# Kernel tuning notes

Measured on AMD Instinct MI355X. Metric: run time of the kernel, lower is better.

The kernel has to match this reference:

```python
import jax, jax.numpy as jnp
import numpy as np

N = 50000      # nodes
E = 800000     # edges
IN = 128       # in_channels
HID = 32       # hidden_channels (per-head dim)
HEADS = 4
HC = HEADS * HID  # 128
OUT = 16       # classes
B = 64         # graphs in batch


def setup_inputs() -> dict:
    key = jax.random.key(0)
    ks = jax.random.split(key, 32)
    def nrm(k, shp, scale):
        return (jax.random.normal(k, shp, jnp.float32) * scale).astype(jnp.float32)
    inp = {}
    inp["x"] = nrm(ks[0], (N, IN), 1.0)
    inp["edge_index"] = jax.random.randint(ks[1], (2, E), 0, N, dtype=jnp.int32)
    inp["edge_attr"] = nrm(ks[2], (E, HID), 1.0)
    inp["batch"] = jnp.sort(jax.random.randint(ks[3], (N,), 0, B, dtype=jnp.int32))
    s_in = IN ** -0.5
    s_hc = HC ** -0.5
    s_hid = HID ** -0.5
    # conv1: lin_query/key/value (IN->HC, bias), lin_edge (HID->HC, no bias), lin_skip (IN->HC, bias)
    inp["wq1"] = nrm(ks[4], (IN, HC), s_in);  inp["bq1"] = jnp.zeros((HC,), jnp.float32)
    inp["wk1"] = nrm(ks[5], (IN, HC), s_in);  inp["bk1"] = jnp.zeros((HC,), jnp.float32)
    inp["wv1"] = nrm(ks[6], (IN, HC), s_in);  inp["bv1"] = jnp.zeros((HC,), jnp.float32)
    inp["we1"] = nrm(ks[7], (HID, HC), s_hid)
    inp["ws1"] = nrm(ks[8], (IN, HC), s_in);  inp["bs1"] = jnp.zeros((HC,), jnp.float32)
    # conv2: input dim HC
    inp["wq2"] = nrm(ks[9], (HC, HC), s_hc);  inp["bq2"] = jnp.zeros((HC,), jnp.float32)
    inp["wk2"] = nrm(ks[10], (HC, HC), s_hc); inp["bk2"] = jnp.zeros((HC,), jnp.float32)
    inp["wv2"] = nrm(ks[11], (HC, HC), s_hc); inp["bv2"] = jnp.zeros((HC,), jnp.float32)
    inp["we2"] = nrm(ks[12], (HID, HC), s_hid)
    inp["ws2"] = nrm(ks[13], (HC, HC), s_hc); inp["bs2"] = jnp.zeros((HC,), jnp.float32)
    # final classifier
    inp["wlin"] = nrm(ks[14], (HC, OUT), s_hc); inp["blin"] = jnp.zeros((OUT,), jnp.float32)
    return inp


def _tconv(x, src, tgt, ea, wq, bq, wk, bk, wv, bv, we, ws, bs):
    """PyG TransformerConv (concat=True, root_weight=True, eval/no dropout)."""
    qn = x @ wq + bq          # [N, HC]
    kn = x @ wk + bk
    vn = x @ wv + bv
    e = ea @ we               # [E, HC] edge embedding (added to key and value)
    q = qn[tgt].reshape(E, HEADS, HID)
    k = (kn[src] + e).reshape(E, HEADS, HID)
    v = (vn[src] + e).reshape(E, HEADS, HID)
    alpha = (q * k).sum(-1) / np.float32(np.sqrt(HID))   # [E, HEADS]
    # segment softmax over target node
    m = jax.ops.segment_max(alpha, tgt, num_segments=N)  # [N, HEADS]
    a = jnp.exp(alpha - m[tgt])
    den = jax.ops.segment_sum(a, tgt, num_segments=N)
    a = a / den[tgt]
    agg = jax.ops.segment_sum(a[:, :, None] * v, tgt, num_segments=N)  # [N, HEADS, HID]
    return agg.reshape(N, HC) + (x @ ws + bs)


def reference(x, edge_index, edge_attr, batch,
              wq1, bq1, wk1, bk1, wv1, bv1, we1, ws1, bs1,
              wq2, bq2, wk2, bk2, wv2, bv2, we2, ws2, bs2,
              wlin, blin):
    src, tgt = edge_index[0], edge_index[1]
    h = jax.nn.elu(_tconv(x, src, tgt, edge_attr, wq1, bq1, wk1, bk1, wv1, bv1, we1, ws1, bs1))
    h = jax.nn.elu(_tconv(h, src, tgt, edge_attr, wq2, bq2, wk2, bk2, wv2, bv2, we2, ws2, bs2))
    # global mean pool over graphs
    s = jax.ops.segment_sum(h, batch, num_segments=B)                    # [B, HC]
    cnt = jax.ops.segment_sum(jnp.ones((N,), jnp.float32), batch, num_segments=B)
    pooled = s / jnp.maximum(cnt, 1.0)[:, None]
    logits = pooled @ wlin + blin
    return jax.nn.log_softmax(logits, axis=-1)
```

## Files before the change

### kernel.cpp

```cpp
#include <hip/hip_runtime.h>
#include <hip/hip_fp16.h>

#define N_NODES 50000
#define N_EDGES 800000
#define IN_C 128
#define HID 32
#define HC 128
#define OUT_C 16
#define NGRAPH 64
#define PNB 125
#define TPB 2

typedef __attribute__((ext_vector_type(8))) _Float16 half8;
typedef __attribute__((ext_vector_type(4))) _Float16 half4v;
typedef __attribute__((ext_vector_type(2))) _Float16 half2v;
typedef __attribute__((ext_vector_type(4))) float floatx4;

__global__ void k_hist(const int* __restrict__ tgt, int* __restrict__ deg) {
  int i = blockIdx.x * blockDim.x + threadIdx.x;
  if (i < N_EDGES) atomicAdd(&deg[tgt[i]], 1);
}

__global__ __launch_bounds__(1024) void k_scan(const int* __restrict__ deg,
                                               int* __restrict__ offs,
                                               int* __restrict__ cursor) {
  __shared__ int wsum[16];
  __shared__ int carry_s;
  int lane = threadIdx.x & 63, wid = threadIdx.x >> 6;
  if (threadIdx.x == 0) { carry_s = 0; offs[0] = 0; }
  __syncthreads();
  for (int base = 0; base < N_NODES; base += 1024) {
    int i = base + threadIdx.x;
    int v = (i < N_NODES) ? deg[i] : 0;
    int x = v;
#pragma unroll
    for (int off = 1; off < 64; off <<= 1) {
      int t = __shfl_up(x, off, 64);
      if (lane >= off) x += t;
    }
    if (lane == 63) wsum[wid] = x;
    __syncthreads();
    if (wid == 0 && lane < 16) {
      int s = wsum[lane];
#pragma unroll
      for (int off = 1; off < 16; off <<= 1) {
        int t = __shfl_up(s, off, 64);
        if (lane >= off) s += t;
      }
      wsum[lane] = s;
    }
    __syncthreads();
    int add = (wid > 0 ? wsum[wid - 1] : 0) + carry_s;
    int incl = x + add;
    if (i < N_NODES) { offs[i + 1] = incl; cursor[i] = incl - v; }
    __syncthreads();
    if (threadIdx.x == 1023) carry_s = incl;
    __syncthreads();
  }
}

__global__ void k_scatter(const int* __restrict__ src, const int* __restrict__ tgt,
                          int* __restrict__ cursor, int* __restrict__ srcs,
                          int* __restrict__ eids) {
  int i = blockIdx.x * blockDim.x + threadIdx.x;
  if (i < N_EDGES) {
    int pos = atomicAdd(&cursor[tgt[i]], 1);
    srcs[pos] = src[i];
    eids[pos] = i;
  }
}

__global__ __launch_bounds__(256) void k_perm_ea(const int* __restrict__ eids,
                                                 const float* __restrict__ ea,
                                                 _Float16* __restrict__ eac) {
  int i = blockIdx.x * 32 + (threadIdx.x >> 3);
  int c = (threadIdx.x & 7) * 4;
  if (i < N_EDGES) {
    float4 v = *(const float4*)&ea[(size_t)eids[i] * HID + c];
    half4v h = {(_Float16)v.x, (_Float16)v.y, (_Float16)v.z, (_Float16)v.w};
    *(half4v*)&eac[(size_t)i * HID + c] = h;
  }
}

__global__ void k_conv_x(const float* __restrict__ x, _Float16* __restrict__ x16) {
  int i = blockIdx.x * 256 + threadIdx.x;
  if (i * 8 < N_NODES * HC) {
    float4 v0 = *(const float4*)&x[i * 8];
    float4 v1 = *(const float4*)&x[i * 8 + 4];
    half8 h = {(_Float16)v0.x, (_Float16)v0.y, (_Float16)v0.z, (_Float16)v0.w,
               (_Float16)v1.x, (_Float16)v1.y, (_Float16)v1.z, (_Float16)v1.w};
    *(half8*)&x16[i * 8] = h;
  }
}

__global__ __launch_bounds__(128) void k_conv_w(
    const float* __restrict__ wq, const float* __restrict__ wk,
    const float* __restrict__ wv, const float* __restrict__ ws,
    _Float16* __restrict__ wt) {
  int g = blockIdx.x;
  int k = threadIdx.x;
  const float* w = (g < 128) ? wq : (g < 256) ? wk : (g < 384) ? wv : ws;
  int c = g & 127;
  wt[g * HC + k] = (_Float16)w[k * HC + c];
}

__global__ __launch_bounds__(128) void k_fold_p(const float* __restrict__ wq,
                                                const float* __restrict__ bq,
                                                const float* __restrict__ we,
                                                _Float16* __restrict__ wt,
                                                float* __restrict__ bp) {
  int c = blockIdx.x;
  int k = threadIdx.x;
  int hb = (c >> 5) << 5, j = c & 31;
  float s = 0.f;
#pragma unroll
  for (int d = 0; d < 32; ++d)
    s = fmaf(wq[k * HC + hb + d], we[j * HC + hb + d], s);
  wt[(size_t)(512 + c) * HC + k] = (_Float16)s;
  if (k == 0) {
    float b = 0.f;
    for (int d = 0; d < 32; ++d) b = fmaf(bq[hb + d], we[j * HC + hb + d], b);
    bp[c] = b;
  }
}

__global__ __launch_bounds__(256) void k_gemm(
    const _Float16* __restrict__ ain,
    const _Float16* __restrict__ wt,
    const float* __restrict__ bq, const float* __restrict__ bk,
    const float* __restrict__ bv, const float* __restrict__ bs,
    const float* __restrict__ bp,
    __half* __restrict__ qn16, _Float16* __restrict__ kv16,
    float* __restrict__ sk, __half* __restrict__ p16) {
  __shared__ _Float16 Bs[128][132];
  int tid = threadIdx.x;
  int wv = tid >> 6, lane = tid & 63;
  int quad = lane >> 4, l16 = lane & 15;
  int cb = blockIdx.y;

#pragma unroll
  for (int i = 0; i < 8; ++i) {
    int chunk = i * 256 + tid;
    int col = chunk >> 4, kc16 = chunk & 15;
    half8 b = *(const half8*)&wt[(size_t)(cb * 128 + col) * HC + kc16 * 8];
    *(half8*)&Bs[col][kc16 * 8] = b;
  }

  int r0 = blockIdx.x * 128 + wv * 32;
  half8 A[2][4];
#pragma unroll
  for (int m = 0; m < 2; ++m) {
    int arow = min(r0 + m * 16 + l16, N_NODES - 1);
#pragma unroll
    for (int kc = 0; kc < 4; ++kc)
      A[m][kc] = *(const half8*)&ain[(size_t)arow * HC + kc * 32 + quad * 8];
  }
  floatx4 acc[8][2];
#pragma unroll
  for (int ct = 0; ct < 8; ++ct) {
    acc[ct][0] = (floatx4){0.f, 0.f, 0.f, 0.f};
    acc[ct][1] = (floatx4){0.f, 0.f, 0.f, 0.f};
  }
  __syncthreads();

#pragma unroll
  for (int ct = 0; ct < 8; ++ct) {
#pragma unroll
    for (int kc = 0; kc < 4; ++kc) {
      half8 B = *(const half8*)&Bs[ct * 16 + l16][kc * 32 + quad * 8];
      acc[ct][0] = __builtin_amdgcn_mfma_f32_16x16x32_f16(A[0][kc], B, acc[ct][0], 0, 0, 0);
      acc[ct][1] = __builtin_amdgcn_mfma_f32_16x16x32_f16(A[1][kc], B, acc[ct][1], 0, 0, 0);
    }
  }

  const float* bias = (cb == 0) ? bq : (cb == 1) ? bk : (cb == 2) ? bv
                    : (cb == 3) ? bs : bp;
#pragma unroll
  for (int ct = 0; ct < 8; ++ct) {
    int lc = (ct << 4) + l16;
    float b = bias[lc];
#pragma unroll
    for (int m = 0; m < 2; ++m) {
#pragma unroll
      for (int reg = 0; reg < 4; ++reg) {
        int row = r0 + m * 16 + quad * 4 + reg;
        if (row < N_NODES) {
          float val = acc[ct][m][reg] + b;
          if (cb == 0) qn16[(size_t)row * HC + lc] = __float2half(val);
          else if (cb == 1) kv16[(size_t)row * 256 + lc] = (_Float16)val;
          else if (cb == 2) kv16[(size_t)row * 256 + 128 + lc] = (_Float16)val;
          else if (cb == 3) sk[(size_t)row * HC + lc] = val;
          else p16[(size_t)row * HC + lc] = __float2half(val);
        }
      }
    }
  }
}

__device__ __forceinline__ float dot8(half8 a, half8 b, float c) {
#if __has_builtin(__builtin_amdgcn_fdot2)
#pragma unroll
  for (int i = 0; i < 4; ++i) {
    half2v x = {a[2 * i], a[2 * i + 1]};
    half2v y = {b[2 * i], b[2 * i + 1]};
    c = __builtin_amdgcn_fdot2(x, y, c, false);
  }
#else
#pragma unroll
  for (int i = 0; i < 8; ++i) c = fmaf((float)a[i], (float)b[i], c);
#endif
  return c;
}

__device__ __forceinline__ float quad_red(float x) {
  int b = __builtin_amdgcn_update_dpp(0, __float_as_int(x), 0xB1, 0xF, 0xF, true);
  float y = x + __int_as_float(b);
  int c2 = __builtin_amdgcn_update_dpp(0, __float_as_int(y), 0x4E, 0xF, 0xF, true);
  return y + __int_as_float(c2);
}

__global__ __launch_bounds__(128) void k_edge_attn(
    const int* __restrict__ offs, const int* __restrict__ srcs,
    const _Float16* __restrict__ eac,
    const _Float16* __restrict__ qn, const _Float16* __restrict__ kv,
    const float* __restrict__ sk,
    const _Float16* __restrict__ pn, const float* __restrict__ we,
    float* __restrict__ out, _Float16* __restrict__ o16) {
  int lane = threadIdx.x & 63;
  int wv_ = threadIdx.x >> 6;
  int t = blockIdx.x * TPB + wv_;
  int g = lane >> 4;
  int p = lane & 15;
  int f0 = p << 3;
  int jd0 = (p & 3) << 3;

  half8 qh = *(const half8*)&qn[(size_t)t * HC + f0];
  half8 ph = *(const half8*)&pn[(size_t)t * HC + ((p >> 2) << 5) + jd0];

  int e0 = offs[t], e1 = offs[t + 1];
  const float inv_sqrt = 0.17677669529663687f;
  float den = 0.f;
  float acc[8], tac[8];
#pragma unroll
  for (int i = 0; i < 8; ++i) { acc[i] = 0.f; tac[i] = 0.f; }

  int sl = (e0 < e1) ? srcs[min(e0 + (lane & 15), e1 - 1)] : 0;
  for (int base = e0; base < e1; base += 16) {
    int cnt = e1 - base;
    half8 K[4], V[4], E[4];
#pragma unroll
    for (int i = 0; i < 4; ++i) {
      int j = 4 * g + i;
      int jc = min(j, cnt - 1);
      int s = __shfl(sl, jc, 64);
      const _Float16* kvp = &kv[(size_t)s * 256];
      K[i] = *(const half8*)&kvp[f0];
      V[i] = *(const half8*)&kvp[128 + f0];
      E[i] = *(const half8*)&eac[(size_t)(base + jc) * HID + jd0];
    }
    int nb = base + 16;
    int sl_n = (nb < e1) ? srcs[min(nb + (lane & 15), e1 - 1)] : 0;
#pragma unroll
    for (int i = 0; i < 4; ++i) {
      int j = 4 * g + i;
      float part = dot8(qh, K[i], 0.f);
      part = dot8(ph, E[i], part);
      part = quad_red(part);
      float w = (j < cnt) ? __expf(part * inv_sqrt) : 0.f;
      den += w;
#pragma unroll
      for (int q2 = 0; q2 < 8; ++q2) {
        acc[q2] = fmaf(w, (float)V[i][q2], acc[q2]);
        tac[q2] = fmaf(w, (float)E[i][q2], tac[q2]);
      }
    }
    sl = sl_n;
  }

#pragma unroll
  for (int i = 0; i < 8; ++i) {
    acc[i] += __shfl_xor(acc[i], 16, 64); acc[i] += __shfl_xor(acc[i], 32, 64);
    tac[i] += __shfl_xor(tac[i], 16, 64); tac[i] += __shfl_xor(tac[i], 32, 64);
  }
  den += __shfl_xor(den, 16, 64);
  den += __shfl_xor(den, 32, 64);

  __shared__ float tl[TPB][16][9];
  if (g == 0) {
#pragma unroll
    for (int i = 0; i < 8; ++i) tl[wv_][p][i] = tac[i];
  }
  float fx[8];
#pragma unroll
  for (int i = 0; i < 8; ++i) fx[i] = 0.f;
  int r = (p & 12) + g;
#pragma unroll
  for (int u = 0; u < 8; ++u) {
    float tv = tl[wv_][r][u];
    int j = (g << 3) + u;
    const float4* wr = (const float4*)&we[j * HC + f0];
    float4 w0 = wr[0], w1 = wr[1];
    fx[0] = fmaf(tv, w0.x, fx[0]); fx[1] = fmaf(tv, w0.y, fx[1]);
    fx[2] = fmaf(tv, w0.z, fx[2]); fx[3] = fmaf(tv, w0.w, fx[3]);
    fx[4] = fmaf(tv, w1.x, fx[4]); fx[5] = fmaf(tv, w1.y, fx[5]);
    fx[6] = fmaf(tv, w1.z, fx[6]); fx[7] = fmaf(tv, w1.w, fx[7]);
  }
#pragma unroll
  for (int i = 0; i < 8; ++i) {
    fx[i] += __shfl_xor(fx[i], 16, 64);
    fx[i] += __shfl_xor(fx[i], 32, 64);
  }

  if (g == 0) {
    float rd = (e1 > e0) ? (1.0f / den) : 0.f;
    const float4* skp = (const float4*)&sk[(size_t)t * HC + f0];
    float4 sa = skp[0], sb = skp[1];
    float o[8];
    o[0] = fmaf(acc[0] + fx[0], rd, sa.x);
    o[1] = fmaf(acc[1] + fx[1], rd, sa.y);
    o[2] = fmaf(acc[2] + fx[2], rd, sa.z);
    o[3] = fmaf(acc[3] + fx[3], rd, sa.w);
    o[4] = fmaf(acc[4] + fx[4], rd, sb.x);
    o[5] = fmaf(acc[5] + fx[5], rd, sb.y);
    o[6] = fmaf(acc[6] + fx[6], rd, sb.z);
    o[7] = fmaf(acc[7] + fx[7], rd, sb.w);
#pragma unroll
    for (int i = 0; i < 8; ++i) o[i] = o[i] > 0.f ? o[i] : __expf(o[i]) - 1.f;
    *(float4*)&out[(size_t)t * HC + f0] = (float4){o[0], o[1], o[2], o[3]};
    *(float4*)&out[(size_t)t * HC + f0 + 4] = (float4){o[4], o[5], o[6], o[7]};
    half8 v16 = {(_Float16)o[0], (_Float16)o[1], (_Float16)o[2], (_Float16)o[3],
                 (_Float16)o[4], (_Float16)o[5], (_Float16)o[6], (_Float16)o[7]};
    *(half8*)&o16[(size_t)t * HC + f0] = v16;
  }
}

__global__ __launch_bounds__(128) void k_pool_sum(const float* __restrict__ h,
                                                  const int* __restrict__ batch,
                                                  float* __restrict__ psum) {
  int c = threadIdx.x;
  int n0 = blockIdx.x * PNB;
  int n1 = n0 + PNB;
  float acc = 0.f;
  int curb = batch[n0];
  for (int n = n0; n < n1; ++n) {
    int b = batch[n];
    if (b != curb) {
      atomicAdd(&psum[curb * HC + c], acc);
      acc = 0.f;
      curb = b;
    }
    acc += h[n * HC + c];
  }
  atomicAdd(&psum[curb * HC + c], acc);
}

__global__ __launch_bounds__(1024) void k_classify(const float* __restrict__ psum,
                                                   const int* __restrict__ batch,
                                                   const float* __restrict__ wlin,
                                                   const float* __restrict__ blin,
                                                   float* __restrict__ out) {
  int tid = threadIdx.x;
  int b = tid >> 4, o = tid & 15;
  int lo = 0, hi = N_NODES;
  while (lo < hi) { int mid = (lo + hi) >> 1; if (batch[mid] < b) lo = mid + 1; else hi = mid; }
  int start = lo;
  lo = 0; hi = N_NODES;
  while (lo < hi) { int mid = (lo + hi) >> 1; if (batch[mid] <= b) lo = mid + 1; else hi = mid; }
  float cnt = fmaxf((float)(lo - start), 1.0f);
  float dot = 0.f;
  for (int d = 0; d < HC; ++d) dot = fmaf(psum[b * HC + d], wlin[d * OUT_C + o], dot);
  float acc = dot / cnt + blin[o];
  float mx = acc;
#pragma unroll
  for (int off = 8; off > 0; off >>= 1) mx = fmaxf(mx, __shfl_xor(mx, off, 64));
  float ex = __expf(acc - mx);
  float sum = ex;
#pragma unroll
  for (int off = 8; off > 0; off >>= 1) sum += __shfl_xor(sum, off, 64);
  out[tid] = acc - mx - logf(sum);
}

extern "C" void kernel_launch(void* const* d_in, const int* in_sizes, int n_in,
                              void* d_out, int out_size, void* d_ws, size_t ws_size,
                              hipStream_t stream) {
  const float* x = (const float*)d_in[0];
  const int* ei = (const int*)d_in[1];
  const float* ea = (const float*)d_in[2];
  const int* batch = (const int*)d_in[3];
  const float* wq1 = (const float*)d_in[4];  const float* bq1 = (const float*)d_in[5];
  const float* wk1 = (const float*)d_in[6];  const float* bk1 = (const float*)d_in[7];
  const float* wv1 = (const float*)d_in[8];  const float* bv1 = (const float*)d_in[9];
  const float* we1 = (const float*)d_in[10];
  const float* ws1 = (const float*)d_in[11]; const float* bs1 = (const float*)d_in[12];
  const float* wq2 = (const float*)d_in[13]; const float* bq2 = (const float*)d_in[14];
  const float* wk2 = (const float*)d_in[15]; const float* bk2 = (const float*)d_in[16];
  const float* wv2 = (const float*)d_in[17]; const float* bv2 = (const float*)d_in[18];
  const float* we2 = (const float*)d_in[19];
  const float* ws2 = (const float*)d_in[20]; const float* bs2 = (const float*)d_in[21];
  const float* wlin = (const float*)d_in[22]; const float* blin = (const float*)d_in[23];

  const int* srcI = ei;
  const int* tgtI = ei + N_EDGES;

  char* wsb = (char*)d_ws;
  size_t off = 0;
  auto alloc = [&](size_t bytes) -> void* {
    void* ptr = wsb + off;
    off += (bytes + 255) & ~(size_t)255;
    return ptr;
  };
  __half* qn16 = (__half*)alloc((size_t)N_NODES * HC * 2);
  _Float16* kv16 = (_Float16*)alloc((size_t)N_NODES * 256 * 2);
  __half* p16  = (__half*)alloc((size_t)N_NODES * HC * 2);
  float* sk = (float*)alloc((size_t)N_NODES * HC * 4);
  float* h  = (float*)alloc((size_t)N_NODES * HC * 4);
  _Float16* in16 = (_Float16*)alloc((size_t)N_NODES * HC * 2);
  _Float16* wt1 = (_Float16*)alloc((size_t)640 * HC * 2);
  _Float16* wt2 = (_Float16*)alloc((size_t)640 * HC * 2);
  float* bp1 = (float*)alloc((size_t)HC * 4);
  float* bp2 = (float*)alloc((size_t)HC * 4);
  float* psum = (float*)alloc((size_t)NGRAPH * HC * 4);
  int* deg    = (int*)alloc((size_t)N_NODES * 4);
  int* offs   = (int*)alloc((size_t)(N_NODES + 1) * 4);
  int* cursor = (int*)alloc((size_t)N_NODES * 4);
  int* srcs   = (int*)alloc((size_t)N_EDGES * 4);
  int* eids   = (int*)alloc((size_t)N_EDGES * 4);
  _Float16* eac = (_Float16*)alloc((size_t)N_EDGES * HID * 2);

  hipMemsetAsync(deg, 0, (size_t)N_NODES * 4, stream);
  k_hist<<<(N_EDGES + 255) / 256, 256, 0, stream>>>(tgtI, deg);
  k_scan<<<1, 1024, 0, stream>>>(deg, offs, cursor);
  k_scatter<<<(N_EDGES + 255) / 256, 256, 0, stream>>>(srcI, tgtI, cursor, srcs, eids);
  k_perm_ea<<<N_EDGES / 32, 256, 0, stream>>>(eids, ea, eac);

  k_conv_x<<<(N_NODES * HC / 8 + 255) / 256, 256, 0, stream>>>(x, in16);
  k_conv_w<<<512, 128, 0, stream>>>(wq1, wk1, wv1, ws1, wt1);
  k_conv_w<<<512, 128, 0, stream>>>(wq2, wk2, wv2, ws2, wt2);
  k_fold_p<<<128, 128, 0, stream>>>(wq1, bq1, we1, wt1, bp1);
  k_fold_p<<<128, 128, 0, stream>>>(wq2, bq2, we2, wt2, bp2);

  dim3 gemm_grid((N_NODES + 127) / 128, 5);
  k_gemm<<<gemm_grid, 256, 0, stream>>>(in16, wt1, bq1, bk1, bv1, bs1, bp1,
                                        qn16, kv16, sk, p16);
  k_edge_attn<<<N_NODES / TPB, 64 * TPB, 0, stream>>>(
      offs, srcs, eac, (const _Float16*)qn16, kv16, sk,
      (const _Float16*)p16, we1, h, in16);
  k_gemm<<<gemm_grid, 256, 0, stream>>>(in16, wt2, bq2, bk2, bv2, bs2, bp2,
                                        qn16, kv16, sk, p16);
  k_edge_attn<<<N_NODES / TPB, 64 * TPB, 0, stream>>>(
      offs, srcs, eac, (const _Float16*)qn16, kv16, sk,
      (const _Float16*)p16, we2, h, in16);

  hipMemsetAsync(psum, 0, (size_t)NGRAPH * HC * 4, stream);
  k_pool_sum<<<N_NODES / PNB, 128, 0, stream>>>(h, batch, psum);
  k_classify<<<1, 1024, 0, stream>>>(psum, batch, wlin, blin, (float*)d_out);
}
```

Before: 704.9 us.

## Fuse edge scatter with attribute permute and store skip/output in fp16

Merges the CSR scatter and edge-attribute permutation into one kernel. Eight lanes share a single atomic slot via shuffle, which removes the eids array and the indirect gather of ea. The skip projection and the layer output are now stored as fp16 instead of fp32, and the redundant fp32 h write is dropped, with pooling reading the fp16 output. This cuts global memory traffic at the cost of more rounding in the skip term and pooled features.

```diff
diff --git a/kernel.cpp b/kernel.cpp
--- a/kernel.cpp
+++ b/kernel.cpp
@@ -59,27 +59,20 @@
   }
 }
 
-__global__ void k_scatter(const int* __restrict__ src, const int* __restrict__ tgt,
-                          int* __restrict__ cursor, int* __restrict__ srcs,
-                          int* __restrict__ eids) {
-  int i = blockIdx.x * blockDim.x + threadIdx.x;
-  if (i < N_EDGES) {
-    int pos = atomicAdd(&cursor[tgt[i]], 1);
-    srcs[pos] = src[i];
-    eids[pos] = i;
-  }
-}
-
-__global__ __launch_bounds__(256) void k_perm_ea(const int* __restrict__ eids,
-                                                 const float* __restrict__ ea,
-                                                 _Float16* __restrict__ eac) {
+__global__ __launch_bounds__(256) void k_scatter(
+    const int* __restrict__ src, const int* __restrict__ tgt,
+    int* __restrict__ cursor, const float* __restrict__ ea,
+    int* __restrict__ srcs, _Float16* __restrict__ eac) {
   int i = blockIdx.x * 32 + (threadIdx.x >> 3);
-  int c = (threadIdx.x & 7) * 4;
-  if (i < N_EDGES) {
-    float4 v = *(const float4*)&ea[(size_t)eids[i] * HID + c];
-    half4v h = {(_Float16)v.x, (_Float16)v.y, (_Float16)v.z, (_Float16)v.w};
-    *(half4v*)&eac[(size_t)i * HID + c] = h;
-  }
+  int c = threadIdx.x & 7;
+  int lane = threadIdx.x & 63;
+  int pos = 0;
+  if (c == 0) pos = atomicAdd(&cursor[tgt[i]], 1);
+  pos = __shfl(pos, lane & 0x38, 64);
+  if (c == 0) srcs[pos] = src[i];
+  float4 v = *(const float4*)&ea[(size_t)i * HID + c * 4];
+  half4v h = {(_Float16)v.x, (_Float16)v.y, (_Float16)v.z, (_Float16)v.w};
+  *(half4v*)&eac[(size_t)pos * HID + c * 4] = h;
 }
 
 __global__ void k_conv_x(const float* __restrict__ x, _Float16* __restrict__ x16) {
@@ -131,7 +124,7 @@
     const float* __restrict__ bv, const float* __restrict__ bs,
     const float* __restrict__ bp,
     __half* __restrict__ qn16, _Float16* __restrict__ kv16,
-    float* __restrict__ sk, __half* __restrict__ p16) {
+    _Float16* __restrict__ sk16, __half* __restrict__ p16) {
   __shared__ _Float16 Bs[128][132];
   int tid = threadIdx.x;
   int wv = tid >> 6, lane = tid & 63;
@@ -189,7 +182,7 @@
           if (cb == 0) qn16[(size_t)row * HC + lc] = __float2half(val);
           else if (cb == 1) kv16[(size_t)row * 256 + lc] = (_Float16)val;
           else if (cb == 2) kv16[(size_t)row * 256 + 128 + lc] = (_Float16)val;
-          else if (cb == 3) sk[(size_t)row * HC + lc] = val;
+          else if (cb == 3) sk16[(size_t)row * HC + lc] = (_Float16)val;
           else p16[(size_t)row * HC + lc] = __float2half(val);
         }
       }
@@ -223,9 +216,9 @@
     const int* __restrict__ offs, const int* __restrict__ srcs,
     const _Float16* __restrict__ eac,
     const _Float16* __restrict__ qn, const _Float16* __restrict__ kv,
-    const float* __restrict__ sk,
+    const _Float16* __restrict__ sk,
     const _Float16* __restrict__ pn, const float* __restrict__ we,
-    float* __restrict__ out, _Float16* __restrict__ o16) {
+    _Float16* __restrict__ o16) {
   int lane = threadIdx.x & 63;
   int wv_ = threadIdx.x >> 6;
   int t = blockIdx.x * TPB + wv_;
@@ -313,28 +306,20 @@
 
   if (g == 0) {
     float rd = (e1 > e0) ? (1.0f / den) : 0.f;
-    const float4* skp = (const float4*)&sk[(size_t)t * HC + f0];
-    float4 sa = skp[0], sb = skp[1];
+    half8 s8 = *(const half8*)&sk[(size_t)t * HC + f0];
     float o[8];
-    o[0] = fmaf(acc[0] + fx[0], rd, sa.x);
-    o[1] = fmaf(acc[1] + fx[1], rd, sa.y);
-    o[2] = fmaf(acc[2] + fx[2], rd, sa.z);
-    o[3] = fmaf(acc[3] + fx[3], rd, sa.w);
-    o[4] = fmaf(acc[4] + fx[4], rd, sb.x);
-    o[5] = fmaf(acc[5] + fx[5], rd, sb.y);
-    o[6] = fmaf(acc[6] + fx[6], rd, sb.z);
-    o[7] = fmaf(acc[7] + fx[7], rd, sb.w);
-#pragma unroll
-    for (int i = 0; i < 8; ++i) o[i] = o[i] > 0.f ? o[i] : __expf(o[i]) - 1.f;
-    *(float4*)&out[(size_t)t * HC + f0] = (float4){o[0], o[1], o[2], o[3]};
-    *(float4*)&out[(size_t)t * HC + f0 + 4] = (float4){o[4], o[5], o[6], o[7]};
+#pragma unroll
+    for (int i = 0; i < 8; ++i) {
+      o[i] = fmaf(acc[i] + fx[i], rd, (float)s8[i]);
+      o[i] = o[i] > 0.f ? o[i] : __expf(o[i]) - 1.f;
+    }
     half8 v16 = {(_Float16)o[0], (_Float16)o[1], (_Float16)o[2], (_Float16)o[3],
                  (_Float16)o[4], (_Float16)o[5], (_Float16)o[6], (_Float16)o[7]};
     *(half8*)&o16[(size_t)t * HC + f0] = v16;
   }
 }
 
-__global__ __launch_bounds__(128) void k_pool_sum(const float* __restrict__ h,
+__global__ __launch_bounds__(128) void k_pool_sum(const _Float16* __restrict__ h16,
                                                   const int* __restrict__ batch,
                                                   float* __restrict__ psum) {
   int c = threadIdx.x;
@@ -349,7 +334,7 @@
       acc = 0.f;
       curb = b;
     }
-    acc += h[n * HC + c];
+    acc += (float)h16[(size_t)n * HC + c];
   }
   atomicAdd(&psum[curb * HC + c], acc);
 }
@@ -412,8 +397,8 @@
   __half* qn16 = (__half*)alloc((size_t)N_NODES * HC * 2);
   _Float16* kv16 = (_Float16*)alloc((size_t)N_NODES * 256 * 2);
   __half* p16  = (__half*)alloc((size_t)N_NODES * HC * 2);
-  float* sk = (float*)alloc((size_t)N_NODES * HC * 4);
-  float* h  = (float*)alloc((size_t)N_NODES * HC * 4);
+  _Float16* sk16 = (_Float16*)alloc((size_t)N_NODES * HC * 2);
+  _Float16* h16 = (_Float16*)alloc((size_t)N_NODES * HC * 2);
   _Float16* in16 = (_Float16*)alloc((size_t)N_NODES * HC * 2);
   _Float16* wt1 = (_Float16*)alloc((size_t)640 * HC * 2);
   _Float16* wt2 = (_Float16*)alloc((size_t)640 * HC * 2);
@@ -424,14 +409,12 @@
   int* offs   = (int*)alloc((size_t)(N_NODES + 1) * 4);
   int* cursor = (int*)alloc((size_t)N_NODES * 4);
   int* srcs   = (int*)alloc((size_t)N_EDGES * 4);
-  int* eids   = (int*)alloc((size_t)N_EDGES * 4);
   _Float16* eac = (_Float16*)alloc((size_t)N_EDGES * HID * 2);
 
   hipMemsetAsync(deg, 0, (size_t)N_NODES * 4, stream);
   k_hist<<<(N_EDGES + 255) / 256, 256, 0, stream>>>(tgtI, deg);
   k_scan<<<1, 1024, 0, stream>>>(deg, offs, cursor);
-  k_scatter<<<(N_EDGES + 255) / 256, 256, 0, stream>>>(srcI, tgtI, cursor, srcs, eids);
-  k_perm_ea<<<N_EDGES / 32, 256, 0, stream>>>(eids, ea, eac);
+  k_scatter<<<N_EDGES / 32, 256, 0, stream>>>(srcI, tgtI, cursor, ea, srcs, eac);
 
   k_conv_x<<<(N_NODES * HC / 8 + 255) / 256, 256, 0, stream>>>(x, in16);
   k_conv_w<<<512, 128, 0, stream>>>(wq1, wk1, wv1, ws1, wt1);
@@ -441,17 +424,17 @@
 
   dim3 gemm_grid((N_NODES + 127) / 128, 5);
   k_gemm<<<gemm_grid, 256, 0, stream>>>(in16, wt1, bq1, bk1, bv1, bs1, bp1,
-                                        qn16, kv16, sk, p16);
+                                        qn16, kv16, sk16, p16);
   k_edge_attn<<<N_NODES / TPB, 64 * TPB, 0, stream>>>(
-      offs, srcs, eac, (const _Float16*)qn16, kv16, sk,
-      (const _Float16*)p16, we1, h, in16);
+      offs, srcs, eac, (const _Float16*)qn16, kv16, sk16,
+      (const _Float16*)p16, we1, in16);
   k_gemm<<<gemm_grid, 256, 0, stream>>>(in16, wt2, bq2, bk2, bv2, bs2, bp2,
-                                        qn16, kv16, sk, p16);
+                                        qn16, kv16, sk16, p16);
   k_edge_attn<<<N_NODES / TPB, 64 * TPB, 0, stream>>>(
-      offs, srcs, eac, (const _Float16*)qn16, kv16, sk,
-      (const _Float16*)p16, we2, h, in16);
+      offs, srcs, eac, (const _Float16*)qn16, kv16, sk16,
+      (const _Float16*)p16, we2, h16);
 
   hipMemsetAsync(psum, 0, (size_t)NGRAPH * HC * 4, stream);
-  k_pool_sum<<<N_NODES / PNB, 128, 0, stream>>>(h, batch, psum);
+  k_pool_sum<<<N_NODES / PNB, 128, 0, stream>>>(h16, batch, psum);
   k_classify<<<1, 1024, 0, stream>>>(psum, batch, wlin, blin, (float*)d_out);
 }
```

Measured after the change: 662.3 us. 1.06x faster.
